# Kernel optimization log

Hardware: AMD Instinct MI355X
Metric: run time of the kernel (lower is better)

## Reference

```python
import jax, jax.numpy as jnp
import numpy as np

IMG = 448; P = 16; C = 3; D = 512; DC = 8; DS = 4
NH = IMG // P            # 28 patches per side
NPATCH = NH * NH         # 784
PDIM = C * P * P         # 768
BATCH = 32
EPS = 1e-5


def setup_inputs() -> dict:
    key = jax.random.key(0)
    ks = jax.random.split(key, 10)
    def lin(k, fan_in, shape):
        bound = 1.0 / np.sqrt(fan_in)
        return jax.random.uniform(k, shape, jnp.float32, -bound, bound)
    return {
        "images": jax.random.normal(ks[0], (BATCH, C, IMG, IMG), jnp.float32),
        "W_patch": lin(ks[1], PDIM, (PDIM, D)),
        "b_patch": jnp.zeros((D,), jnp.float32),
        "pos_embed": jax.random.normal(ks[2], (1, NPATCH, D), jnp.float32) * 0.02,
        "W_coord": lin(ks[3], D, (D, DC)),
        "b_coord": jnp.zeros((DC,), jnp.float32),
        "W_spinor": lin(ks[4], D, (D, DS)),
        "b_spinor": jnp.zeros((DS,), jnp.float32),
        "W_embed": lin(ks[5], DC, (DC, D)),
        "b_embed": jnp.zeros((D,), jnp.float32),
        "ln_gamma": jnp.ones((D,), jnp.float32),
        "ln_beta": jnp.zeros((D,), jnp.float32),
        "W_out": lin(ks[6], D, (D, D)),
        "b_out": jnp.zeros((D,), jnp.float32),
    }


def reference(images, W_patch, b_patch, pos_embed, W_coord, b_coord,
              W_spinor, b_spinor, W_embed, b_embed,
              ln_gamma, ln_beta, W_out, b_out):
    B = images.shape[0]
    # patchify == F.unfold(kernel=stride=P).transpose(1,2):
    # patches[b, bh*NH+bw, c*P*P + i*P + j] = images[b, c, bh*P+i, bw*P+j]
    patches = images.reshape(B, C, NH, P, NH, P)
    patches = patches.transpose(0, 2, 4, 1, 3, 5).reshape(B, NPATCH, PDIM)
    # patch embed + positional embedding  -> (B, NPATCH, D)
    x = patches @ W_patch + b_patch + pos_embed
    # manifold projection: coords (B,N,DC), spinor (B,N,DS)
    coords = x @ W_coord + b_coord
    spinor = x @ W_spinor + b_spinor
    # K0 scalar bilinear: psi^T psi -> (B, N)
    K0 = jnp.sum(spinor * spinor, axis=-1)
    # embed back from manifold coords -> (B, N, D)
    x_manifold = coords @ W_embed + b_embed
    # K0-modulated remix + residual
    x_enh = x_manifold * K0[..., None] + x
    # output projection: LayerNorm -> Linear
    mu = jnp.mean(x_enh, axis=-1, keepdims=True)
    var = jnp.mean(jnp.square(x_enh - mu), axis=-1, keepdims=True)
    x_norm = (x_enh - mu) * jax.lax.rsqrt(var + EPS) * ln_gamma + ln_beta
    return x_norm @ W_out + b_out
```

## Files before the change

### kernel.cpp

```cpp
#include <hip/hip_runtime.h>
#include <hip/hip_bf16.h>
#include <stdint.h>


typedef __bf16 bf16_t;
typedef bf16_t bf16x8 __attribute__((ext_vector_type(8)));
typedef bf16_t bf16x4 __attribute__((ext_vector_type(4)));
typedef float  f32x4  __attribute__((ext_vector_type(4)));

#define IMG     448
#define PSZ     16
#define NHP     28
#define NPATCH  784
#define PDIM    768
#define DMODEL  512
#define MROWS   25088

__device__ __forceinline__ void gload16(void* lds, const void* g) {
  __builtin_amdgcn_global_load_lds(
      (__attribute__((address_space(1))) void*)(uintptr_t)g,
      (__attribute__((address_space(3))) void*)lds,
      16, 0, 0);
}

__device__ __forceinline__ unsigned short bfbits(float v) {
  bf16_t h = (bf16_t)v;
  unsigned short u;
  __builtin_memcpy(&u, &h, 2);
  return u;
}
__device__ __forceinline__ float f_from_bits(unsigned u) {
  float f; __builtin_memcpy(&f, &u, 4); return f;
}

__global__ __launch_bounds__(256) void transpose_to_bf16(
    const float* __restrict__ src, bf16_t* __restrict__ dst, int K, int N)
{
  __shared__ float t[64][65];
  const int tx = threadIdx.x;
  const int ty = threadIdx.y;
  const int bx = blockIdx.x * 64;
  const int by = blockIdx.y * 64;
  #pragma unroll
  for (int r = ty; r < 64; r += 4)
    t[r][tx] = src[(size_t)(by + r) * N + (bx + tx)];
  __syncthreads();
  #pragma unroll
  for (int r = ty; r < 64; r += 4)
    dst[(size_t)(bx + r) * K + (by + tx)] = (bf16_t)t[tx][r];
}

__global__ __launch_bounds__(256) void manifold_prep(
    const float* __restrict__ Wc, const float* __restrict__ Ws,
    const float* __restrict__ We, const float* __restrict__ be,
    bf16_t* __restrict__ Wcsg, bf16_t* __restrict__ Wcs2g, bf16_t* __restrict__ Wetg)
{
  const int idx = blockIdx.x * 256 + threadIdx.x;
  if (idx < 8192) {
    const int r = idx >> 9, n = idx & 511;
    float v;
    if (r < 8)       v = Wc[n * 8 + r];
    else if (r < 12) v = Ws[n * 4 + (r - 8)];
    else { const float f = Ws[n * 4 + (r - 12)]; v = f - (float)(bf16_t)f; }
    Wcsg[idx] = (bf16_t)v;
  } else if (idx < 12288) {
    const int j = idx - 8192;
    const int r = j >> 9, n = j & 511;
    const float f = Wc[n * 8 + r];
    Wcs2g[j] = (bf16_t)(f - (float)(bf16_t)f);
  } else if (idx < 24576) {
    const int j = idx - 12288;
    const int n = j / 24, k = j % 24;
    float v = 0.f;
    if (k < 16)      v = We[(k & 7) * 512 + n];
    else if (k == 16) v = be[n];
    else if (k == 17) { const float f = be[n]; v = f - (float)(bf16_t)f; }
    Wetg[j] = (bf16_t)v;
  }
}

__global__ __launch_bounds__(256) void patchify_bf16(
    const float* __restrict__ images, bf16_t* __restrict__ Apat)
{
  __shared__ bf16_t t[16][456];
  const int tid = threadIdx.x;
  const int bid = blockIdx.x;
  const int b = bid / 84, rem = bid % 84;
  const int c = rem / 28, ph = rem % 28;
  const float* src = images + ((size_t)(b * 3 + c) * IMG + ph * PSZ) * IMG;

  #pragma unroll
  for (int idx = tid; idx < 16 * 112; idx += 256) {
    const int i = idx / 112, x4 = idx % 112;
    const float4 v = *(const float4*)(src + (size_t)i * IMG + x4 * 4);
    bf16x4 w;
    w[0] = (bf16_t)v.x; w[1] = (bf16_t)v.y; w[2] = (bf16_t)v.z; w[3] = (bf16_t)v.w;
    *(bf16x4*)&t[i][x4 * 4] = w;
  }
  __syncthreads();

  const size_t mbase = (size_t)b * NPATCH + (size_t)ph * NHP;
  #pragma unroll
  for (int idx = tid; idx < 28 * 64; idx += 256) {
    const int pw = idx >> 6, e = idx & 63;
    const int i = e >> 2, j4 = e & 3;
    const bf16x4 w = *(const bf16x4*)&t[i][pw * 16 + j4 * 4];
    *(bf16x4*)&Apat[(mbase + pw) * PDIM + c * 256 + i * 16 + j4 * 4] = w;
  }
}

template<int KDIM, int EPI>
__global__ __launch_bounds__(256) void gemm_bf16(
    const bf16_t* __restrict__ A, const bf16_t* __restrict__ BT,
    const float* __restrict__ bias, const float* __restrict__ pos,
    void* __restrict__ outp)
{
  __shared__ bf16_t As[128][32];
  __shared__ bf16_t Bs[128][32];

  const int tid  = threadIdx.x;
  const int orig = blockIdx.x;
  const int wg   = (orig & 7) * 98 + (orig >> 3);
  const int n0   = (wg & 3) * 128;
  const int m0   = (wg >> 2) * 128;

  const int wave = tid >> 6, lane = tid & 63;
  const int rsub = lane >> 2;
  const int cb   = (lane & 3) * 8;

  const bf16_t* agp0 = A  + ((size_t)(m0 + 32 * wave) + rsub)      * KDIM + cb;
  const bf16_t* agp1 = A  + ((size_t)(m0 + 32 * wave) + 16 + rsub) * KDIM + cb;
  const bf16_t* bgp0 = BT + ((size_t)(n0 + 32 * wave) + rsub)      * KDIM + cb;
  const bf16_t* bgp1 = BT + ((size_t)(n0 + 32 * wave) + 16 + rsub) * KDIM + cb;
  bf16_t* alds0 = &As[32 * wave][0];
  bf16_t* alds1 = &As[32 * wave + 16][0];
  bf16_t* blds0 = &Bs[32 * wave][0];
  bf16_t* blds1 = &Bs[32 * wave + 16][0];

  const int wm = (wave >> 1) << 6;
  const int wn = (wave & 1) << 6;
  const int lr = lane & 15;
  const int lk = (lane >> 4) << 3;

  f32x4 acc[4][4] = {};

  for (int k0 = 0; k0 < KDIM; k0 += 32) {
    __syncthreads();
    gload16(alds0, agp0 + k0);
    gload16(alds1, agp1 + k0);
    gload16(blds0, bgp0 + k0);
    gload16(blds1, bgp1 + k0);
    __syncthreads();

    bf16x8 af[4], bfr[4];
    #pragma unroll
    for (int i = 0; i < 4; ++i) af[i]  = *(const bf16x8*)&As[wm + i * 16 + lr][lk];
    #pragma unroll
    for (int j = 0; j < 4; ++j) bfr[j] = *(const bf16x8*)&Bs[wn + j * 16 + lr][lk];
    #pragma unroll
    for (int i = 0; i < 4; ++i)
      #pragma unroll
      for (int j = 0; j < 4; ++j)
        acc[i][j] = __builtin_amdgcn_mfma_f32_16x16x32_bf16(af[i], bfr[j], acc[i][j], 0, 0, 0);
  }

  const int q4 = (lane >> 4) << 2;
  const int colb = n0 + wn;
  #pragma unroll
  for (int i = 0; i < 4; ++i) {
    #pragma unroll
    for (int r = 0; r < 4; ++r) {
      const int mm = m0 + wm + i * 16 + q4 + r;
      if (EPI == 0) {
        const int pp = mm % NPATCH;
        const float* pe = pos + (size_t)pp * DMODEL;
        bf16_t* orow = (bf16_t*)outp + (size_t)mm * DMODEL;
        #pragma unroll
        for (int j = 0; j < 4; ++j) {
          const int nn = colb + j * 16 + lr;
          orow[nn] = (bf16_t)(acc[i][j][r] + bias[nn] + pe[nn]);
        }
      } else {
        float* orow = (float*)outp + (size_t)mm * DMODEL;
        #pragma unroll
        for (int j = 0; j < 4; ++j) {
          const int nn = colb + j * 16 + lr;
          orow[nn] = acc[i][j][r] + bias[nn];
        }
      }
    }
  }
}

__global__ __launch_bounds__(256) void gemm1_fused_fallback(
    const float* __restrict__ images, const bf16_t* __restrict__ WpT,
    const float* __restrict__ b_patch, const float* __restrict__ pos_embed,
    bf16_t* __restrict__ xout)
{
  __shared__ bf16_t As[128][40];
  __shared__ bf16_t Bs[128][40];
  const int tid = threadIdx.x;
  const int n0 = blockIdx.x * 128;
  const int m0 = blockIdx.y * 128;
  const int sr = tid >> 1;
  const int sh = tid & 1;
  const int m  = m0 + sr;
  const int b  = m / NPATCH;
  const int p  = m - b * NPATCH;
  const int ph = p / NHP;
  const int pw = p - ph * NHP;
  const float* abase = images + (size_t)(b * 3) * (IMG * IMG)
                              + (size_t)(ph * PSZ) * IMG + pw * PSZ;
  const bf16_t* brow = WpT + (size_t)(n0 + sr) * PDIM + sh * 16;
  const int wave = tid >> 6;
  const int lane = tid & 63;
  const int wm = (wave >> 1) << 6;
  const int wn = (wave & 1) << 6;
  const int lr = lane & 15;
  const int lk = (lane >> 4) << 3;
  f32x4 acc[4][4] = {};
  for (int ks = 0; ks < PDIM / 32; ++ks) {
    const int k0 = ks * 32;
    const int c  = k0 >> 8;
    const int ib = (k0 >> 4) & 15;
    const float* asrc = abase + (size_t)c * (IMG * IMG) + (ib + sh) * IMG;
    const float4 av0 = *(const float4*)(asrc + 0);
    const float4 av1 = *(const float4*)(asrc + 4);
    const float4 av2 = *(const float4*)(asrc + 8);
    const float4 av3 = *(const float4*)(asrc + 12);
    const uint4 bv0 = *(const uint4*)(brow + k0);
    const uint4 bv1 = *(const uint4*)(brow + k0 + 8);
    __syncthreads();
    bf16x8 a0, a1;
    a0[0] = (bf16_t)av0.x; a0[1] = (bf16_t)av0.y; a0[2] = (bf16_t)av0.z; a0[3] = (bf16_t)av0.w;
    a0[4] = (bf16_t)av1.x; a0[5] = (bf16_t)av1.y; a0[6] = (bf16_t)av1.z; a0[7] = (bf16_t)av1.w;
    a1[0] = (bf16_t)av2.x; a1[1] = (bf16_t)av2.y; a1[2] = (bf16_t)av2.z; a1[3] = (bf16_t)av2.w;
    a1[4] = (bf16_t)av3.x; a1[5] = (bf16_t)av3.y; a1[6] = (bf16_t)av3.z; a1[7] = (bf16_t)av3.w;
    *(bf16x8*)&As[sr][sh * 16]     = a0;
    *(bf16x8*)&As[sr][sh * 16 + 8] = a1;
    *(uint4*)&Bs[sr][sh * 16]      = bv0;
    *(uint4*)&Bs[sr][sh * 16 + 8]  = bv1;
    __syncthreads();
    bf16x8 af[4], bfr[4];
    #pragma unroll
    for (int i = 0; i < 4; ++i) af[i]  = *(const bf16x8*)&As[wm + i * 16 + lr][lk];
    #pragma unroll
    for (int j = 0; j < 4; ++j) bfr[j] = *(const bf16x8*)&Bs[wn + j * 16 + lr][lk];
    #pragma unroll
    for (int i = 0; i < 4; ++i)
      #pragma unroll
      for (int j = 0; j < 4; ++j)
        acc[i][j] = __builtin_amdgcn_mfma_f32_16x16x32_bf16(af[i], bfr[j], acc[i][j], 0, 0, 0);
  }
  const int colb = n0 + wn;
  #pragma unroll
  for (int i = 0; i < 4; ++i) {
    #pragma unroll
    for (int r = 0; r < 4; ++r) {
      const int mm = m0 + wm + i * 16 + ((lane >> 4) << 2) + r;
      const int pp = mm % NPATCH;
      const float* pe = pos_embed + (size_t)pp * DMODEL;
      bf16_t* orow = xout + (size_t)mm * DMODEL;
      #pragma unroll
      for (int j = 0; j < 4; ++j) {
        const int nn = colb + j * 16 + lr;
        orow[nn] = (bf16_t)(acc[i][j][r] + b_patch[nn] + pe[nn]);
      }
    }
  }
}

__global__ __launch_bounds__(256) void manifold_ln_v3(
    bf16_t* __restrict__ x,
    const bf16_t* __restrict__ Wcsg, const bf16_t* __restrict__ Wcs2g,
    const bf16_t* __restrict__ Wetg,
    const float* __restrict__ b_coord, const float* __restrict__ b_spinor,
    const float* __restrict__ ln_gamma, const float* __restrict__ ln_beta)
{
  __shared__ bf16_t sWcs[16 * 512];
  __shared__ bf16_t sWcs2[8 * 512];
  __shared__ bf16_t sWeT[512 * 24];
  __shared__ float  cT[4][16][12];
  __shared__ bf16_t sg[512], sb[512];

  const int tid = threadIdx.x;

  #pragma unroll
  for (int i = 0; i < 4; ++i) {
    const int c = tid + 256 * i;
    const int r = c >> 6, off = (c & 63) * 16;
    const uint4 v = *(const uint4*)((const char*)Wcsg + (size_t)c * 16);
    *(uint4*)((char*)sWcs + ((r * 1024 + off) ^ ((r & 7) << 4))) = v;
  }
  #pragma unroll
  for (int i = 0; i < 2; ++i) {
    const int c = tid + 256 * i;
    const int r = c >> 6, off = (c & 63) * 16;
    const uint4 v = *(const uint4*)((const char*)Wcs2g + (size_t)c * 16);
    *(uint4*)((char*)sWcs2 + ((r * 1024 + off) ^ ((r & 7) << 4))) = v;
  }
  #pragma unroll
  for (int i = 0; i < 6; ++i) {
    const int c = tid + 256 * i;
    *(uint4*)((char*)sWeT + (size_t)c * 16) =
        *(const uint4*)((const char*)Wetg + (size_t)c * 16);
  }
  for (int i = tid; i < 512; i += 256) {
    sg[i] = (bf16_t)ln_gamma[i];
    sb[i] = (bf16_t)ln_beta[i];
  }
  __syncthreads();

  const int w    = tid >> 6;
  const int lane = tid & 63;
  const int lr   = lane & 15;
  const int lk   = (lane >> 4) << 3;
  const int q4   = (lane >> 4) << 2;
  const int m0w  = blockIdx.x * 64 + w * 16;

  const float bcs = (lr < 8) ? b_coord[lr] : (lr < 12 ? b_spinor[lr - 8] : 0.f);

  const bf16_t* xrow = x + (size_t)(m0w + lr) * DMODEL + lk;
  f32x4 acc1  = {0.f, 0.f, 0.f, 0.f};
  f32x4 acc1b = {0.f, 0.f, 0.f, 0.f};
  const bf16_t zb = (bf16_t)0.f;
  #pragma unroll
  for (int ks = 0; ks < 16; ++ks) {
    const bf16x8 af = *(const bf16x8*)(xrow + ks * 32);
    const int wb = (lr * 1024 + ks * 64 + lk * 2) ^ ((lr & 7) << 4);
    const bf16x8 w1 = *(const bf16x8*)((const char*)sWcs + wb);
    acc1 = __builtin_amdgcn_mfma_f32_16x16x32_bf16(af, w1, acc1, 0, 0, 0);
    bf16x8 w2 = {zb, zb, zb, zb, zb, zb, zb, zb};
    if (lr < 8) w2 = *(const bf16x8*)((const char*)sWcs2 + wb);
    acc1b = __builtin_amdgcn_mfma_f32_16x16x32_bf16(af, w2, acc1b, 0, 0, 0);
  }

  float k0r[4], svals[4];
  #pragma unroll
  for (int r = 0; r < 4; ++r) {
    const float s = acc1[r] + acc1b[r] + bcs;
    svals[r] = s;
    if (lr < 8) cT[w][q4 + r][lr] = s;
  }
  #pragma unroll
  for (int r = 0; r < 4; ++r) {
    const float sp = svals[r] + __shfl_xor(svals[r], 4, 64);
    float sq = (lr >= 8 && lr < 12) ? sp * sp : 0.f;
    sq += __shfl_xor(sq, 1, 64);
    sq += __shfl_xor(sq, 2, 64);
    sq += __shfl_xor(sq, 4, 64);
    sq += __shfl_xor(sq, 8, 64);
    k0r[r] = sq;
  }
  __syncthreads();

  const f32x4 c0 = *(const f32x4*)&cT[w][lr][0];
  const f32x4 c4 = *(const f32x4*)&cT[w][lr][4];
  const bf16_t oneb = (bf16_t)1.0f;
  bf16x8 a2;
  #pragma unroll
  for (int j = 0; j < 8; ++j) {
    const float cv = (j < 4) ? c0[j] : c4[j - 4];
    const bf16_t hi = (bf16_t)cv;
    const bf16_t lo = (bf16_t)(cv - (float)hi);
    bf16_t v;
    if (lk == 0)       v = hi;
    else if (lk == 8)  v = lo;
    else if (lk == 16) v = (j < 2) ? oneb : zb;
    else               v = zb;
    a2[j] = v;
  }

  const bf16_t* xres = x + (size_t)(m0w + q4) * DMODEL + lr;
  unsigned xp[4][16];
  float s1[4] = {0.f, 0.f, 0.f, 0.f};
  float s2[4] = {0.f, 0.f, 0.f, 0.f};
  const int woff = (lk & 16) ? 32 : lk * 2;
  #pragma unroll
  for (int j = 0; j < 32; ++j) {
    const int n = j * 16 + lr;
    bf16x8 wf = *(const bf16x8*)((const char*)sWeT + n * 48 + woff);
    if (lk == 24) {
      #pragma unroll
      for (int t = 0; t < 8; ++t) wf[t] = zb;
    }
    f32x4 acc2 = {0.f, 0.f, 0.f, 0.f};
    acc2 = __builtin_amdgcn_mfma_f32_16x16x32_bf16(a2, wf, acc2, 0, 0, 0);
    #pragma unroll
    for (int r = 0; r < 4; ++r) {
      const float xg = (float)xres[(size_t)r * DMODEL + j * 16];
      const float xe = acc2[r] * k0r[r] + xg;
      s1[r] += xe;
      s2[r] += xe * xe;
      const unsigned short ub = bfbits(xe);
      if ((j & 1) == 0) xp[r][j >> 1] = ub;
      else              xp[r][j >> 1] |= ((unsigned)ub) << 16;
    }
  }

  float mu[4], rsg[4];
  #pragma unroll
  for (int r = 0; r < 4; ++r) {
    float a = s1[r], b2 = s2[r];
    #pragma unroll
    for (int off = 1; off <= 8; off <<= 1) {
      a  += __shfl_xor(a, off, 64);
      b2 += __shfl_xor(b2, off, 64);
    }
    const float m = a * (1.f / 512.f);
    const float v = b2 * (1.f / 512.f) - m * m;
    mu[r]  = m;
    rsg[r] = rsqrtf(v + 1e-5f);
  }

  bf16_t* xo = x + (size_t)(m0w + q4) * DMODEL;
  #pragma unroll
  for (int jp = 0; jp < 16; ++jp) {
    const int n0 = jp * 32 + lr, n1 = n0 + 16;
    const float g0 = (float)sg[n0], bb0 = (float)sb[n0];
    const float g1 = (float)sg[n1], bb1 = (float)sb[n1];
    #pragma unroll
    for (int r = 0; r < 4; ++r) {
      const unsigned p = xp[r][jp];
      const float flo = f_from_bits(p << 16);
      const float fhi = f_from_bits(p & 0xffff0000u);
      const float o0 = (flo - mu[r]) * rsg[r] * g0 + bb0;
      const float o1 = (fhi - mu[r]) * rsg[r] * g1 + bb1;
      xo[(size_t)r * DMODEL + n0] = (bf16_t)o0;
      xo[(size_t)r * DMODEL + n1] = (bf16_t)o1;
    }
  }
}

extern "C" void kernel_launch(void* const* d_in, const int* in_sizes, int n_in,
                              void* d_out, int out_size, void* d_ws, size_t ws_size,
                              hipStream_t stream)
{
  const float* images    = (const float*)d_in[0];
  const float* W_patch   = (const float*)d_in[1];
  const float* b_patch   = (const float*)d_in[2];
  const float* pos_embed = (const float*)d_in[3];
  const float* W_coord   = (const float*)d_in[4];
  const float* b_coord   = (const float*)d_in[5];
  const float* W_spinor  = (const float*)d_in[6];
  const float* b_spinor  = (const float*)d_in[7];
  const float* W_embed   = (const float*)d_in[8];
  const float* b_embed   = (const float*)d_in[9];
  const float* ln_gamma  = (const float*)d_in[10];
  const float* ln_beta   = (const float*)d_in[11];
  const float* W_out     = (const float*)d_in[12];
  const float* b_out     = (const float*)d_in[13];
  float* out = (float*)d_out;

  const size_t SZ_APAT = (size_t)MROWS * PDIM * 2;
  const size_t SZ_X    = (size_t)MROWS * DMODEL * 2;
  const size_t SZ_WPT  = (size_t)DMODEL * PDIM * 2;
  const size_t SZ_WOT  = (size_t)DMODEL * DMODEL * 2;
  const size_t SZ_WCS  = 16 * 512 * 2;
  const size_t SZ_WCS2 = 8 * 512 * 2;
  const size_t SZ_WET  = 512 * 24 * 2;
  const size_t NEED_FULL = SZ_APAT + SZ_X + SZ_WPT + SZ_WOT + SZ_WCS + SZ_WCS2 + SZ_WET;

  char* ws = (char*)d_ws;
  const bool full = (ws_size >= NEED_FULL);

  bf16_t *Apat, *x, *WpT, *WoT, *Wcsg, *Wcs2g, *Wetg;
  if (full) {
    char* p = ws;
    Apat  = (bf16_t*)p;            p += SZ_APAT;
    x     = (bf16_t*)p;            p += SZ_X;
    WpT   = (bf16_t*)p;            p += SZ_WPT;
    WoT   = (bf16_t*)p;            p += SZ_WOT;
    Wcsg  = (bf16_t*)p;            p += SZ_WCS;
    Wcs2g = (bf16_t*)p;            p += SZ_WCS2;
    Wetg  = (bf16_t*)p;
  } else {
    char* p = ws;
    Apat  = nullptr;
    x     = (bf16_t*)p;            p += SZ_X;
    WpT   = (bf16_t*)p;            p += SZ_WPT;
    WoT   = (bf16_t*)p;            p += SZ_WOT;
    Wcsg  = (bf16_t*)p;            p += SZ_WCS;
    Wcs2g = (bf16_t*)p;            p += SZ_WCS2;
    Wetg  = (bf16_t*)p;
  }

  hipLaunchKernelGGL(transpose_to_bf16, dim3(8, 12), dim3(64, 4), 0, stream,
                     W_patch, WpT, PDIM, DMODEL);
  hipLaunchKernelGGL(transpose_to_bf16, dim3(8, 8), dim3(64, 4), 0, stream,
                     W_out, WoT, DMODEL, DMODEL);
  hipLaunchKernelGGL(manifold_prep, dim3(96), dim3(256), 0, stream,
                     W_coord, W_spinor, W_embed, b_embed, Wcsg, Wcs2g, Wetg);

  if (full) {
    hipLaunchKernelGGL(patchify_bf16, dim3(32 * 3 * 28), dim3(256), 0, stream,
                       images, Apat);
    hipLaunchKernelGGL((gemm_bf16<PDIM, 0>), dim3(784), dim3(256), 0, stream,
                       Apat, WpT, b_patch, pos_embed, (void*)x);
  } else {
    hipLaunchKernelGGL(gemm1_fused_fallback, dim3(4, 196), dim3(256), 0, stream,
                       images, WpT, b_patch, pos_embed, x);
  }

  hipLaunchKernelGGL(manifold_ln_v3, dim3(392), dim3(256), 0, stream,
                     x, Wcsg, Wcs2g, Wetg, b_coord, b_spinor, ln_gamma, ln_beta);

  hipLaunchKernelGGL((gemm_bf16<DMODEL, 1>), dim3(784), dim3(256), 0, stream,
                     x, WoT, b_out, (const float*)nullptr, (void*)out);
}
```

Baseline: 126.1 us.

## Drop split-bf16 precision terms and transpose MFMA operands in manifold LayerNorm kernel

The manifold/LayerNorm kernel no longer emulates extra precision with hi/lo bf16 splits of the coord/spinor weights, the coords and the embed bias. That removes the second MFMA per k-step and the extra LDS buffers. MFMA operands are swapped so each lane owns a row with four contiguous columns. This removes the LDS transpose and barrier for the coordinates and allows vectorised bf16x4 residual loads and stores, with LN statistics reduced in fewer shuffles. It lowers numerical accuracy of the coord/K0 path and shrinks LDS use, which may raise occupancy.

New measurement: 128.2 us. No clear change (+1.7%).

```diff
diff --git a/kernel.cpp b/kernel.cpp
--- a/kernel.cpp
+++ b/kernel.cpp
@@ -53,29 +53,22 @@
 __global__ __launch_bounds__(256) void manifold_prep(
     const float* __restrict__ Wc, const float* __restrict__ Ws,
     const float* __restrict__ We, const float* __restrict__ be,
-    bf16_t* __restrict__ Wcsg, bf16_t* __restrict__ Wcs2g, bf16_t* __restrict__ Wetg)
+    bf16_t* __restrict__ Wcsg, bf16_t* __restrict__ We2g)
 {
   const int idx = blockIdx.x * 256 + threadIdx.x;
   if (idx < 8192) {
     const int r = idx >> 9, n = idx & 511;
-    float v;
+    float v = 0.f;
     if (r < 8)       v = Wc[n * 8 + r];
     else if (r < 12) v = Ws[n * 4 + (r - 8)];
-    else { const float f = Ws[n * 4 + (r - 12)]; v = f - (float)(bf16_t)f; }
     Wcsg[idx] = (bf16_t)v;
-  } else if (idx < 12288) {
+  } else {
     const int j = idx - 8192;
-    const int r = j >> 9, n = j & 511;
-    const float f = Wc[n * 8 + r];
-    Wcs2g[j] = (bf16_t)(f - (float)(bf16_t)f);
-  } else if (idx < 24576) {
-    const int j = idx - 12288;
-    const int n = j / 24, k = j % 24;
+    const int n = j >> 4, k = j & 15;
     float v = 0.f;
-    if (k < 16)      v = We[(k & 7) * 512 + n];
-    else if (k == 16) v = be[n];
-    else if (k == 17) { const float f = be[n]; v = f - (float)(bf16_t)f; }
-    Wetg[j] = (bf16_t)v;
+    if (k < 8)       v = We[k * 512 + n];
+    else if (k == 8) v = be[n];
+    We2g[j] = (bf16_t)v;
   }
 }
 
@@ -270,18 +263,15 @@
   }
 }
 
-__global__ __launch_bounds__(256) void manifold_ln_v3(
+__global__ __launch_bounds__(256) void manifold_ln_v4(
     bf16_t* __restrict__ x,
-    const bf16_t* __restrict__ Wcsg, const bf16_t* __restrict__ Wcs2g,
-    const bf16_t* __restrict__ Wetg,
+    const bf16_t* __restrict__ Wcsg, const bf16_t* __restrict__ We2g,
     const float* __restrict__ b_coord, const float* __restrict__ b_spinor,
     const float* __restrict__ ln_gamma, const float* __restrict__ ln_beta)
 {
   __shared__ bf16_t sWcs[16 * 512];
-  __shared__ bf16_t sWcs2[8 * 512];
-  __shared__ bf16_t sWeT[512 * 24];
-  __shared__ float  cT[4][16][12];
-  __shared__ bf16_t sg[512], sb[512];
+  __shared__ bf16_t sWe2[512 * 16];
+  __shared__ float  sg[512], sb[512];
 
   const int tid = threadIdx.x;
 
@@ -293,21 +283,15 @@
     *(uint4*)((char*)sWcs + ((r * 1024 + off) ^ ((r & 7) << 4))) = v;
   }
   #pragma unroll
-  for (int i = 0; i < 2; ++i) {
+  for (int i = 0; i < 4; ++i) {
     const int c = tid + 256 * i;
-    const int r = c >> 6, off = (c & 63) * 16;
-    const uint4 v = *(const uint4*)((const char*)Wcs2g + (size_t)c * 16);
-    *(uint4*)((char*)sWcs2 + ((r * 1024 + off) ^ ((r & 7) << 4))) = v;
-  }
-  #pragma unroll
-  for (int i = 0; i < 6; ++i) {
-    const int c = tid + 256 * i;
-    *(uint4*)((char*)sWeT + (size_t)c * 16) =
-        *(const uint4*)((const char*)Wetg + (size_t)c * 16);
+    const int n = c >> 1, half = (c & 1) * 16;
+    const uint4 v = *(const uint4*)((const char*)We2g + (size_t)c * 16);
+    *(uint4*)((char*)sWe2 + ((n * 32 + half) ^ ((n & 3) << 4))) = v;
   }
   for (int i = tid; i < 512; i += 256) {
-    sg[i] = (bf16_t)ln_gamma[i];
-    sb[i] = (bf16_t)ln_beta[i];
+    sg[i] = ln_gamma[i];
+    sb[i] = ln_beta[i];
   }
   __syncthreads();
 
@@ -318,117 +302,96 @@
   const int q4   = (lane >> 4) << 2;
   const int m0w  = blockIdx.x * 64 + w * 16;
 
-  const float bcs = (lr < 8) ? b_coord[lr] : (lr < 12 ? b_spinor[lr - 8] : 0.f);
+  float bbv[4];
+  #pragma unroll
+  for (int r = 0; r < 4; ++r) {
+    if (q4 == 0)      bbv[r] = b_coord[r];
+    else if (q4 == 4) bbv[r] = b_coord[4 + r];
+    else if (q4 == 8) bbv[r] = b_spinor[r];
+    else              bbv[r] = 0.f;
+  }
 
   const bf16_t* xrow = x + (size_t)(m0w + lr) * DMODEL + lk;
-  f32x4 acc1  = {0.f, 0.f, 0.f, 0.f};
-  f32x4 acc1b = {0.f, 0.f, 0.f, 0.f};
+  f32x4 acc1 = {0.f, 0.f, 0.f, 0.f};
+  #pragma unroll
+  for (int ks = 0; ks < 16; ++ks) {
+    const bf16x8 bf = *(const bf16x8*)(xrow + ks * 32);
+    const int wb = (lr * 1024 + ks * 64 + lk * 2) ^ ((lr & 7) << 4);
+    const bf16x8 wf = *(const bf16x8*)((const char*)sWcs + wb);
+    acc1 = __builtin_amdgcn_mfma_f32_16x16x32_bf16(wf, bf, acc1, 0, 0, 0);
+  }
+
+  float sv[4];
+  #pragma unroll
+  for (int r = 0; r < 4; ++r) sv[r] = acc1[r] + bbv[r];
+
+  const float k0own = sv[0] * sv[0] + sv[1] * sv[1] + sv[2] * sv[2] + sv[3] * sv[3];
+  const float k0v = __shfl(k0own, 32 + lr, 64);
+
+  float ov[4];
+  #pragma unroll
+  for (int r = 0; r < 4; ++r) ov[r] = __shfl_xor(sv[r], 16, 64);
+
   const bf16_t zb = (bf16_t)0.f;
-  #pragma unroll
-  for (int ks = 0; ks < 16; ++ks) {
-    const bf16x8 af = *(const bf16x8*)(xrow + ks * 32);
-    const int wb = (lr * 1024 + ks * 64 + lk * 2) ^ ((lr & 7) << 4);
-    const bf16x8 w1 = *(const bf16x8*)((const char*)sWcs + wb);
-    acc1 = __builtin_amdgcn_mfma_f32_16x16x32_bf16(af, w1, acc1, 0, 0, 0);
-    bf16x8 w2 = {zb, zb, zb, zb, zb, zb, zb, zb};
-    if (lr < 8) w2 = *(const bf16x8*)((const char*)sWcs2 + wb);
-    acc1b = __builtin_amdgcn_mfma_f32_16x16x32_bf16(af, w2, acc1b, 0, 0, 0);
-  }
-
-  float k0r[4], svals[4];
-  #pragma unroll
-  for (int r = 0; r < 4; ++r) {
-    const float s = acc1[r] + acc1b[r] + bcs;
-    svals[r] = s;
-    if (lr < 8) cT[w][q4 + r][lr] = s;
-  }
-  #pragma unroll
-  for (int r = 0; r < 4; ++r) {
-    const float sp = svals[r] + __shfl_xor(svals[r], 4, 64);
-    float sq = (lr >= 8 && lr < 12) ? sp * sp : 0.f;
-    sq += __shfl_xor(sq, 1, 64);
-    sq += __shfl_xor(sq, 2, 64);
-    sq += __shfl_xor(sq, 4, 64);
-    sq += __shfl_xor(sq, 8, 64);
-    k0r[r] = sq;
-  }
-  __syncthreads();
-
-  const f32x4 c0 = *(const f32x4*)&cT[w][lr][0];
-  const f32x4 c4 = *(const f32x4*)&cT[w][lr][4];
-  const bf16_t oneb = (bf16_t)1.0f;
-  bf16x8 a2;
-  #pragma unroll
-  for (int j = 0; j < 8; ++j) {
-    const float cv = (j < 4) ? c0[j] : c4[j - 4];
-    const bf16_t hi = (bf16_t)cv;
-    const bf16_t lo = (bf16_t)(cv - (float)hi);
-    bf16_t v;
-    if (lk == 0)       v = hi;
-    else if (lk == 8)  v = lo;
-    else if (lk == 16) v = (j < 2) ? oneb : zb;
-    else               v = zb;
-    a2[j] = v;
-  }
-
-  const bf16_t* xres = x + (size_t)(m0w + q4) * DMODEL + lr;
-  unsigned xp[4][16];
-  float s1[4] = {0.f, 0.f, 0.f, 0.f};
-  float s2[4] = {0.f, 0.f, 0.f, 0.f};
-  const int woff = (lk & 16) ? 32 : lk * 2;
-  #pragma unroll
-  for (int j = 0; j < 32; ++j) {
-    const int n = j * 16 + lr;
-    bf16x8 wf = *(const bf16x8*)((const char*)sWeT + n * 48 + woff);
-    if (lk == 24) {
-      #pragma unroll
-      for (int t = 0; t < 8; ++t) wf[t] = zb;
+  bf16x8 b2;
+  if (lk == 0) {
+    #pragma unroll
+    for (int r = 0; r < 4; ++r) { b2[r] = (bf16_t)sv[r]; b2[4 + r] = (bf16_t)ov[r]; }
+  } else if (lk == 8) {
+    b2[0] = (bf16_t)1.0f;
+    #pragma unroll
+    for (int t = 1; t < 8; ++t) b2[t] = zb;
+  } else {
+    #pragma unroll
+    for (int t = 0; t < 8; ++t) b2[t] = zb;
+  }
+
+  const bf16_t* xres = x + (size_t)(m0w + lr) * DMODEL + q4;
+  unsigned xpA[32], xpB[32];
+  float s1 = 0.f, s2 = 0.f;
+  #pragma unroll
+  for (int nf = 0; nf < 32; ++nf) {
+    const int n = nf * 16 + lr;
+    const int wb = (n * 32 + lk * 2) ^ ((n & 3) << 4);
+    const bf16x8 wf = *(const bf16x8*)((const char*)sWe2 + wb);
+    f32x4 acc2 = {0.f, 0.f, 0.f, 0.f};
+    acc2 = __builtin_amdgcn_mfma_f32_16x16x32_bf16(wf, b2, acc2, 0, 0, 0);
+
+    const bf16x4 xr = *(const bf16x4*)(xres + nf * 16);
+    float xe[4];
+    #pragma unroll
+    for (int r = 0; r < 4; ++r) {
+      xe[r] = acc2[r] * k0v + (float)xr[r];
+      s1 += xe[r];
+      s2 += xe[r] * xe[r];
     }
-    f32x4 acc2 = {0.f, 0.f, 0.f, 0.f};
-    acc2 = __builtin_amdgcn_mfma_f32_16x16x32_bf16(a2, wf, acc2, 0, 0, 0);
-    #pragma unroll
-    for (int r = 0; r < 4; ++r) {
-      const float xg = (float)xres[(size_t)r * DMODEL + j * 16];
-      const float xe = acc2[r] * k0r[r] + xg;
-      s1[r] += xe;
-      s2[r] += xe * xe;
-      const unsigned short ub = bfbits(xe);
-      if ((j & 1) == 0) xp[r][j >> 1] = ub;
-      else              xp[r][j >> 1] |= ((unsigned)ub) << 16;
-    }
-  }
-
-  float mu[4], rsg[4];
-  #pragma unroll
-  for (int r = 0; r < 4; ++r) {
-    float a = s1[r], b2 = s2[r];
-    #pragma unroll
-    for (int off = 1; off <= 8; off <<= 1) {
-      a  += __shfl_xor(a, off, 64);
-      b2 += __shfl_xor(b2, off, 64);
-    }
-    const float m = a * (1.f / 512.f);
-    const float v = b2 * (1.f / 512.f) - m * m;
-    mu[r]  = m;
-    rsg[r] = rsqrtf(v + 1e-5f);
-  }
-
-  bf16_t* xo = x + (size_t)(m0w + q4) * DMODEL;
-  #pragma unroll
-  for (int jp = 0; jp < 16; ++jp) {
-    const int n0 = jp * 32 + lr, n1 = n0 + 16;
-    const float g0 = (float)sg[n0], bb0 = (float)sb[n0];
-    const float g1 = (float)sg[n1], bb1 = (float)sb[n1];
-    #pragma unroll
-    for (int r = 0; r < 4; ++r) {
-      const unsigned p = xp[r][jp];
-      const float flo = f_from_bits(p << 16);
-      const float fhi = f_from_bits(p & 0xffff0000u);
-      const float o0 = (flo - mu[r]) * rsg[r] * g0 + bb0;
-      const float o1 = (fhi - mu[r]) * rsg[r] * g1 + bb1;
-      xo[(size_t)r * DMODEL + n0] = (bf16_t)o0;
-      xo[(size_t)r * DMODEL + n1] = (bf16_t)o1;
-    }
+    xpA[nf] = (unsigned)bfbits(xe[0]) | ((unsigned)bfbits(xe[1]) << 16);
+    xpB[nf] = (unsigned)bfbits(xe[2]) | ((unsigned)bfbits(xe[3]) << 16);
+  }
+
+  s1 += __shfl_xor(s1, 16, 64);
+  s1 += __shfl_xor(s1, 32, 64);
+  s2 += __shfl_xor(s2, 16, 64);
+  s2 += __shfl_xor(s2, 32, 64);
+  const float mu  = s1 * (1.f / 512.f);
+  const float var = s2 * (1.f / 512.f) - mu * mu;
+  const float rsg = rsqrtf(var + 1e-5f);
+
+  bf16_t* xo = x + (size_t)(m0w + lr) * DMODEL + q4;
+  #pragma unroll
+  for (int nf = 0; nf < 32; ++nf) {
+    const f32x4 g = *(const f32x4*)&sg[nf * 16 + q4];
+    const f32x4 b = *(const f32x4*)&sb[nf * 16 + q4];
+    const float v0 = f_from_bits(xpA[nf] << 16);
+    const float v1 = f_from_bits(xpA[nf] & 0xffff0000u);
+    const float v2 = f_from_bits(xpB[nf] << 16);
+    const float v3 = f_from_bits(xpB[nf] & 0xffff0000u);
+    bf16x4 o;
+    o[0] = (bf16_t)((v0 - mu) * rsg * g[0] + b[0]);
+    o[1] = (bf16_t)((v1 - mu) * rsg * g[1] + b[1]);
+    o[2] = (bf16_t)((v2 - mu) * rsg * g[2] + b[2]);
+    o[3] = (bf16_t)((v3 - mu) * rsg * g[3] + b[3]);
+    *(bf16x4*)(xo + nf * 16) = o;
   }
 }
 
@@ -457,14 +420,13 @@
   const size_t SZ_WPT  = (size_t)DMODEL * PDIM * 2;
   const size_t SZ_WOT  = (size_t)DMODEL * DMODEL * 2;
   const size_t SZ_WCS  = 16 * 512 * 2;
-  const size_t SZ_WCS2 = 8 * 512 * 2;
-  const size_t SZ_WET  = 512 * 24 * 2;
-  const size_t NEED_FULL = SZ_APAT + SZ_X + SZ_WPT + SZ_WOT + SZ_WCS + SZ_WCS2 + SZ_WET;
+  const size_t SZ_WE2  = 512 * 16 * 2;
+  const size_t NEED_FULL = SZ_APAT + SZ_X + SZ_WPT + SZ_WOT + SZ_WCS + SZ_WE2;
 
   char* ws = (char*)d_ws;
   const bool full = (ws_size >= NEED_FULL);
 
-  bf16_t *Apat, *x, *WpT, *WoT, *Wcsg, *Wcs2g, *Wetg;
+  bf16_t *Apat, *x, *WpT, *WoT, *Wcsg, *We2g;
   if (full) {
     char* p = ws;
     Apat  = (bf16_t*)p;            p += SZ_APAT;
@@ -472,8 +434,7 @@
     WpT   = (bf16_t*)p;            p += SZ_WPT;
     WoT   = (bf16_t*)p;            p += SZ_WOT;
     Wcsg  = (bf16_t*)p;            p += SZ_WCS;
-    Wcs2g = (bf16_t*)p;            p += SZ_WCS2;
-    Wetg  = (bf16_t*)p;
+    We2g  = (bf16_t*)p;
   } else {
     char* p = ws;
     Apat  = nullptr;
@@ -481,16 +442,15 @@
     WpT   = (bf16_t*)p;            p += SZ_WPT;
     WoT   = (bf16_t*)p;            p += SZ_WOT;
     Wcsg  = (bf16_t*)p;            p += SZ_WCS;
-    Wcs2g = (bf16_t*)p;            p += SZ_WCS2;
-    Wetg  = (bf16_t*)p;
+    We2g  = (bf16_t*)p;
   }
 
   hipLaunchKernelGGL(transpose_to_bf16, dim3(8, 12), dim3(64, 4), 0, stream,
                      W_patch, WpT, PDIM, DMODEL);
   hipLaunchKernelGGL(transpose_to_bf16, dim3(8, 8), dim3(64, 4), 0, stream,
                      W_out, WoT, DMODEL, DMODEL);
-  hipLaunchKernelGGL(manifold_prep, dim3(96), dim3(256), 0, stream,
-                     W_coord, W_spinor, W_embed, b_embed, Wcsg, Wcs2g, Wetg);
+  hipLaunchKernelGGL(manifold_prep, dim3(64), dim3(256), 0, stream,
+                     W_coord, W_spinor, W_embed, b_embed, Wcsg, We2g);
 
   if (full) {
     hipLaunchKernelGGL(patchify_bf16, dim3(32 * 3 * 28), dim3(256), 0, stream,
@@ -502,8 +462,8 @@
                        images, WpT, b_patch, pos_embed, x);
   }
 
-  hipLaunchKernelGGL(manifold_ln_v3, dim3(392), dim3(256), 0, stream,
-                     x, Wcsg, Wcs2g, Wetg, b_coord, b_spinor, ln_gamma, ln_beta);
+  hipLaunchKernelGGL(manifold_ln_v4, dim3(392), dim3(256), 0, stream,
+                     x, Wcsg, We2g, b_coord, b_spinor, ln_gamma, ln_beta);
 
   hipLaunchKernelGGL((gemm_bf16<DMODEL, 1>), dim3(784), dim3(256), 0, stream,
                      x, WoT, b_out, (const float*)nullptr, (void*)out);
```
